# Performance work log

Hardware: AMD Instinct MI355X
Metric: run time of the kernel (lower is better)

## Reference

```python
import jax, jax.numpy as jnp
import numpy as np

HEADS = 8
DIM_HEAD = 64
SCALE = DIM_HEAD ** -0.5
LN_EPS = 1e-5
NEG_INF = -1e30


def layernorm(x, gamma, beta):
    mu = jnp.mean(x, axis=-1, keepdims=True)
    var = jnp.var(x, axis=-1, keepdims=True)
    return (x - mu) * jax.lax.rsqrt(var + LN_EPS) * gamma + beta


def setup_inputs() -> dict:
    key = jax.random.key(0)
    ks = jax.random.split(key, 8)
    b, f, n, d, inner = 8, 8192, 64, 1024, HEADS * DIM_HEAD
    x = jax.random.normal(ks[0], (b, f, d), dtype=jnp.float32)
    latents = jax.random.normal(ks[1], (b, n, d), dtype=jnp.float32)
    key_padding_mask = jax.random.randint(ks[2], (b, f), 0, 2) > 0  # True = padded
    s = 0.02
    return {
        "x": x,
        "latents": latents,
        "key_padding_mask": key_padding_mask,
        "kv_gate": jnp.float32(-4.0),
        "gamma_media": jnp.ones((d,), jnp.float32),
        "beta_media": jnp.zeros((d,), jnp.float32),
        "gamma_lat": jnp.ones((d,), jnp.float32),
        "beta_lat": jnp.zeros((d,), jnp.float32),
        "Wq": jax.random.normal(ks[3], (d, inner), jnp.float32) * s,
        "Wk": jax.random.normal(ks[4], (d, inner), jnp.float32) * s,
        "Wv": jax.random.normal(ks[5], (d, inner), jnp.float32) * s,
        "Wout": jax.random.normal(ks[6], (inner, d), jnp.float32) * s,
    }


def reference(x, latents, key_padding_mask, kv_gate, gamma_media, beta_media,
              gamma_lat, beta_lat, Wq, Wk, Wv, Wout):
    b, f, d = x.shape
    n = latents.shape[1]
    x = layernorm(x, gamma_media, beta_media)
    latents = layernorm(latents, gamma_lat, beta_lat)
    kv = jnp.concatenate((x, latents * kv_gate), axis=1)  # (b, f+n, d)

    q = (latents @ Wq).reshape(b, n, HEADS, DIM_HEAD)       # (b, q, h, d)
    k = (kv @ Wk).reshape(b, f + n, HEADS, DIM_HEAD)        # (b, kv, h, d)
    v = (kv @ Wv).reshape(b, f + n, HEADS, DIM_HEAD)

    sim = jnp.einsum('bqhd,bkhd->bhqk', q * SCALE, k)       # (b, h, n, f+n)
    sim = sim - jax.lax.stop_gradient(jnp.max(sim, axis=-1, keepdims=True))

    valid_feat = ~key_padding_mask                          # (b, f)
    valid_full = jnp.concatenate(
        (valid_feat, jnp.ones((b, n), dtype=bool)), axis=1)  # (b, f+n)
    sim = jnp.where(valid_full[:, None, None, :], sim, NEG_INF)

    attn = jax.nn.softmax(sim, axis=-1)
    out = jnp.einsum('bhqk,bkhd->bqhd', attn, v).reshape(b, n, HEADS * DIM_HEAD)
    return out @ Wout
```

## Files before the change

### kernel.cpp

```cpp
#include <hip/hip_runtime.h>
#include <stdint.h>


#define KVPAD 8448
#define NCHUNK 33

typedef __attribute__((ext_vector_type(8))) short short8;
typedef __attribute__((ext_vector_type(4))) float f32x4;

typedef __attribute__((address_space(1))) void gvoid;
typedef __attribute__((address_space(3))) void lvoid;

__device__ __forceinline__ unsigned short f2bf(float f) {
    union { float f; uint32_t u; } v; v.f = f;
    uint32_t u = v.u;
    u += 0x7fffu + ((u >> 16) & 1u);
    return (unsigned short)(u >> 16);
}

__device__ __forceinline__ void mfma16(f32x4& c, short8 a, short8 b) {
    asm volatile("v_mfma_f32_16x16x32_bf16 %0, %1, %2, %0"
                 : "+v"(c) : "v"(a), "v"(b));
}

__device__ __forceinline__ void gl2lds16(const void* g, void* l) {
    __builtin_amdgcn_global_load_lds((gvoid*)g, (lvoid*)l, 16, 0, 0);
}

__global__ __launch_bounds__(512) void scan_kernel(
    const int* __restrict__ mask, int* __restrict__ pfx, int* __restrict__ cnt)
{
    int b = threadIdx.x >> 6, lane = threadIdx.x & 63;
    int run = 0;
    for (int it = 0; it < 128; it++) {
        int f = it * 64 + lane;
        int valid = (mask[b * 8192 + f] == 0) ? 1 : 0;
        unsigned long long bal = __ballot(valid);
        int excl = __popcll(bal & ((1ull << lane) - 1ull));
        pfx[b * 8192 + f] = run + excl;
        run += (int)__popcll(bal);
    }
    if (lane == 0) cnt[b] = run;
}

__global__ __launch_bounds__(256) void ln_kernel(
    const float* __restrict__ X, const float* __restrict__ latents,
    const int* __restrict__ mask, const int* __restrict__ pfx,
    const float* __restrict__ gm, const float* __restrict__ bm,
    const float* __restrict__ gl, const float* __restrict__ bl,
    unsigned short* __restrict__ x_ln, unsigned short* __restrict__ lat_ln)
{
    int lane = threadIdx.x & 63;
    int row = blockIdx.x * 4 + (threadIdx.x >> 6);
    const float *src, *g, *bet;
    unsigned short* dst;
    if (row < 65536) {
        if (mask[row] != 0) return;
        int b = row >> 13;
        src = X + (size_t)row * 1024;
        dst = x_ln + ((size_t)b * 8192 + pfx[row]) * 1024;
        g = gm; bet = bm;
    } else {
        int r = row - 65536;
        src = latents + (size_t)r * 1024;
        dst = lat_ln + (size_t)r * 1024;
        g = gl; bet = bl;
    }
    const float4* xr = (const float4*)src;
    float4 v[4];
    float s = 0.f, s2 = 0.f;
#pragma unroll
    for (int i = 0; i < 4; i++) {
        v[i] = xr[i * 64 + lane];
        s  += v[i].x + v[i].y + v[i].z + v[i].w;
        s2 += v[i].x*v[i].x + v[i].y*v[i].y + v[i].z*v[i].z + v[i].w*v[i].w;
    }
#pragma unroll
    for (int off = 1; off < 64; off <<= 1) {
        s += __shfl_xor(s, off);
        s2 += __shfl_xor(s2, off);
    }
    float mean = s * (1.0f / 1024.0f);
    float var  = s2 * (1.0f / 1024.0f) - mean * mean;
    float rs = rsqrtf(var + 1e-5f);
    ushort4* yr = (ushort4*)dst;
    const float4* gp = (const float4*)g;
    const float4* bp = (const float4*)bet;
#pragma unroll
    for (int i = 0; i < 4; i++) {
        int c4 = i * 64 + lane;
        float4 gg = gp[c4], bb = bp[c4];
        ushort4 o;
        o.x = f2bf((v[i].x - mean) * rs * gg.x + bb.x);
        o.y = f2bf((v[i].y - mean) * rs * gg.y + bb.y);
        o.z = f2bf((v[i].z - mean) * rs * gg.z + bb.z);
        o.w = f2bf((v[i].w - mean) * rs * gg.w + bb.w);
        yr[c4] = o;
    }
}

__global__ __launch_bounds__(256) void transpose_cvt(
    const float* __restrict__ Wk, const float* __restrict__ Wv,
    const float* __restrict__ Wq, const float* __restrict__ Wout,
    unsigned short* __restrict__ WkvT, unsigned short* __restrict__ WqT,
    unsigned short* __restrict__ WoutT)
{
    __shared__ float t[64][65];
    const float* S; unsigned short* D; int R, C;
    int z = blockIdx.z;
    if (z == 0)      { S = Wk;   D = WkvT;                      R = 1024; C = 512; }
    else if (z == 1) { S = Wv;   D = WkvT + (size_t)512 * 1024; R = 1024; C = 512; }
    else if (z == 2) { S = Wq;   D = WqT;                       R = 1024; C = 512; }
    else             { S = Wout; D = WoutT;                     R = 512;  C = 1024; }
    int r0 = blockIdx.y * 64, c0 = blockIdx.x * 64;
    if (r0 >= R || c0 >= C) return;
#pragma unroll
    for (int i = 0; i < 16; i++) {
        int o = i * 256 + threadIdx.x;
        int rr = o >> 6, cc = o & 63;
        t[rr][cc] = S[(size_t)(r0 + rr) * C + c0 + cc];
    }
    __syncthreads();
#pragma unroll
    for (int i = 0; i < 16; i++) {
        int o = i * 256 + threadIdx.x;
        int cl = o >> 6, rl = o & 63;
        D[(size_t)(c0 + cl) * R + r0 + rl] = f2bf(t[rl][cl]);
    }
}

__global__ __launch_bounds__(256) void gemm_bf16(
    const unsigned short* __restrict__ A, const unsigned short* __restrict__ BT,
    int Kd,
    unsigned short* __restrict__ Ck, float* __restrict__ Cf,
    unsigned short* __restrict__ CvT,
    int nsplit, int ldc, int P, int Sstride, int Ofs, int kvpad,
    float scale_const, const float* __restrict__ scale_ptr,
    const int* __restrict__ cnt)
{
    __shared__ unsigned short a_lds[128 * 64];
    __shared__ unsigned short b_lds[128 * 64];
    int bx = blockIdx.x, by = blockIdx.y;
    if (gridDim.x == 8 && gridDim.y >= 8 && (gridDim.y & 7) == 0) {
        int lid = by * 8 + bx;
        bx = lid & 7;
        by = (lid >> 6) * 8 + ((lid >> 3) & 7);
    }
    size_t rowbase = (size_t)by * 128;
    size_t colbase = (size_t)bx * 128;
    if (cnt) {
        int bq = (int)rowbase / P, rl = (int)rowbase - bq * P;
        if (rl >= cnt[bq]) return;
    }
    int tid = threadIdx.x;
    int lane = tid & 63;
    int wave = tid >> 6;
    int wrow = (wave >> 1) * 64, wcol = (wave & 1) * 64;
    int qd = lane >> 4, cc = lane & 15;

    f32x4 acc[4][4];
#pragma unroll
    for (int mt = 0; mt < 4; mt++)
#pragma unroll
        for (int nt = 0; nt < 4; nt++)
            acc[mt][nt] = (f32x4){0.f, 0.f, 0.f, 0.f};

    int kiters = Kd >> 6;
    for (int kt = 0; kt < kiters; kt++) {
        int k0 = kt << 6;
#pragma unroll
        for (int i = 0; i < 4; i++) {
            int s = i * 256 + tid;
            int m = s >> 3, kc = s & 7;
            int kg = kc ^ (m & 7);
            gl2lds16(A + (rowbase + m) * (size_t)Kd + (k0 + kg * 8), &a_lds[s * 8]);
        }
#pragma unroll
        for (int i = 0; i < 4; i++) {
            int s = i * 256 + tid;
            int m = s >> 3, kc = s & 7;
            int kg = kc ^ (m & 7);
            gl2lds16(BT + (colbase + m) * (size_t)Kd + (k0 + kg * 8), &b_lds[s * 8]);
        }
        __syncthreads();
#pragma unroll
        for (int ks = 0; ks < 2; ks++) {
            short8 af[4], bfr[4];
            int cg = ks * 4 + qd;
#pragma unroll
            for (int mt = 0; mt < 4; mt++) {
                int m = wrow + mt * 16 + cc;
                af[mt] = *(const short8*)&a_lds[(m * 8 + (cg ^ (m & 7))) * 8];
            }
#pragma unroll
            for (int nt = 0; nt < 4; nt++) {
                int n = wcol + nt * 16 + cc;
                bfr[nt] = *(const short8*)&b_lds[(n * 8 + (cg ^ (n & 7))) * 8];
            }
#pragma unroll
            for (int mt = 0; mt < 4; mt++)
#pragma unroll
                for (int nt = 0; nt < 4; nt++)
                    mfma16(acc[mt][nt], af[mt], bfr[nt]);
        }
        __syncthreads();
    }

    float sc = scale_const;
    if (scale_ptr) sc *= *scale_ptr;
#pragma unroll
    for (int mt = 0; mt < 4; mt++) {
        int g0 = (int)rowbase + wrow + mt * 16 + qd * 4;
        int bq = g0 / P, rl = g0 - bq * P;
#pragma unroll
        for (int nt = 0; nt < 4; nt++) {
            int col = (int)colbase + wcol + nt * 16 + cc;
            if (col < nsplit) {
                int idx0 = bq * Sstride + Ofs + rl;
                if (Cf) {
#pragma unroll
                    for (int r = 0; r < 4; r++)
                        Cf[(size_t)(idx0 + r) * ldc + col] = acc[mt][nt][r] * sc;
                } else {
#pragma unroll
                    for (int r = 0; r < 4; r++)
                        Ck[(size_t)(idx0 + r) * ldc + col] = f2bf(acc[mt][nt][r] * sc);
                }
            } else {
                ushort4 pk;
                pk.x = f2bf(acc[mt][nt][0] * sc);
                pk.y = f2bf(acc[mt][nt][1] * sc);
                pk.z = f2bf(acc[mt][nt][2] * sc);
                pk.w = f2bf(acc[mt][nt][3] * sc);
                *(ushort4*)&CvT[((size_t)bq * 512 + (col - nsplit)) * kvpad + Ofs + rl] = pk;
            }
        }
    }
}

__global__ __launch_bounds__(256) void attn_kernel(
    const unsigned short* __restrict__ Kbuf,
    const unsigned short* __restrict__ Vt,
    const unsigned short* __restrict__ Qbuf,
    const int* __restrict__ cnt,
    float* __restrict__ Opart,
    float* __restrict__ Mpart,
    float* __restrict__ Lpart)
{
    __shared__ unsigned short P_lds[64 * 264];
    __shared__ float red_max[4][64];
    __shared__ float red_sum[4][64];
    __shared__ float mrow[64];

    int chunk = blockIdx.x, h = blockIdx.y, b = blockIdx.z;
    int len = 64 + cnt[b];
    int kv0 = chunk * 256;
    if (kv0 >= len) return;

    int tid = threadIdx.x, lane = tid & 63, w = tid >> 6;
    int qd = lane >> 4, cc = lane & 15;
    int pidx = (b * 8 + h) * NCHUNK + chunk;
    int kvw = kv0 + w * 64;

    short8 qf[4][2];
    const unsigned short* Qb = Qbuf + ((size_t)b * 64) * 512 + h * 64;
#pragma unroll
    for (int mt = 0; mt < 4; mt++)
#pragma unroll
        for (int ks = 0; ks < 2; ks++)
            qf[mt][ks] = *(const short8*)&Qb[(size_t)(mt * 16 + cc) * 512 + ks * 32 + qd * 8];

    f32x4 acc[4][4];
#pragma unroll
    for (int mt = 0; mt < 4; mt++)
#pragma unroll
        for (int nt = 0; nt < 4; nt++)
            acc[mt][nt] = (f32x4){0.f, 0.f, 0.f, 0.f};

    const unsigned short* Kb = Kbuf + (size_t)b * KVPAD * 512 + h * 64;
#pragma unroll
    for (int nt = 0; nt < 4; nt++) {
        int kvr = kvw + nt * 16 + cc;
#pragma unroll
        for (int ks = 0; ks < 2; ks++) {
            short8 kf = *(const short8*)&Kb[(size_t)kvr * 512 + ks * 32 + qd * 8];
#pragma unroll
            for (int mt = 0; mt < 4; mt++)
                mfma16(acc[mt][nt], qf[mt][ks], kf);
        }
    }
#pragma unroll
    for (int nt = 0; nt < 4; nt++) {
        int kv = kvw + nt * 16 + cc;
        if (kv >= len) {
#pragma unroll
            for (int mt = 0; mt < 4; mt++)
#pragma unroll
                for (int r = 0; r < 4; r++) acc[mt][nt][r] = -1e30f;
        }
    }
    float vmax[4][4];
#pragma unroll
    for (int mt = 0; mt < 4; mt++)
#pragma unroll
        for (int r = 0; r < 4; r++)
            vmax[mt][r] = fmaxf(fmaxf(acc[mt][0][r], acc[mt][1][r]),
                                fmaxf(acc[mt][2][r], acc[mt][3][r]));
#pragma unroll
    for (int off = 1; off < 16; off <<= 1)
#pragma unroll
        for (int mt = 0; mt < 4; mt++)
#pragma unroll
            for (int r = 0; r < 4; r++)
                vmax[mt][r] = fmaxf(vmax[mt][r], __shfl_xor(vmax[mt][r], off));
    if (cc == 0) {
#pragma unroll
        for (int mt = 0; mt < 4; mt++)
#pragma unroll
            for (int r = 0; r < 4; r++)
                red_max[w][mt * 16 + qd * 4 + r] = vmax[mt][r];
    }
    __syncthreads();
    if (tid < 64)
        mrow[tid] = fmaxf(fmaxf(red_max[0][tid], red_max[1][tid]),
                          fmaxf(red_max[2][tid], red_max[3][tid]));
    __syncthreads();

    float vsum[4][4];
#pragma unroll
    for (int mt = 0; mt < 4; mt++)
#pragma unroll
        for (int r = 0; r < 4; r++) {
            int row = mt * 16 + qd * 4 + r;
            float m = mrow[row];
            float ssum = 0.f;
#pragma unroll
            for (int nt = 0; nt < 4; nt++) {
                float p = __expf(acc[mt][nt][r] - m);
                ssum += p;
                P_lds[row * 264 + w * 64 + nt * 16 + cc] = f2bf(p);
            }
            vsum[mt][r] = ssum;
        }
#pragma unroll
    for (int off = 1; off < 16; off <<= 1)
#pragma unroll
        for (int mt = 0; mt < 4; mt++)
#pragma unroll
            for (int r = 0; r < 4; r++)
                vsum[mt][r] += __shfl_xor(vsum[mt][r], off);
    if (cc == 0) {
#pragma unroll
        for (int mt = 0; mt < 4; mt++)
#pragma unroll
            for (int r = 0; r < 4; r++)
                red_sum[w][mt * 16 + qd * 4 + r] = vsum[mt][r];
    }
    __syncthreads();
    if (tid < 64) {
        Mpart[(size_t)pidx * 64 + tid] = mrow[tid];
        Lpart[(size_t)pidx * 64 + tid] = red_sum[0][tid] + red_sum[1][tid] +
                                         red_sum[2][tid] + red_sum[3][tid];
    }

    f32x4 acco[4];
#pragma unroll
    for (int mt = 0; mt < 4; mt++) acco[mt] = (f32x4){0.f, 0.f, 0.f, 0.f};
    const unsigned short* Vb = Vt + ((size_t)b * 512 + h * 64 + w * 16 + cc) * KVPAD + kv0;
#pragma unroll
    for (int ks = 0; ks < 8; ks++) {
        short8 vf = *(const short8*)&Vb[ks * 32 + qd * 8];
#pragma unroll
        for (int mt = 0; mt < 4; mt++) {
            short8 pf = *(const short8*)&P_lds[(size_t)(mt * 16 + cc) * 264 + ks * 32 + qd * 8];
            mfma16(acco[mt], pf, vf);
        }
    }
    float* Ob = Opart + (size_t)pidx * 4096;
#pragma unroll
    for (int mt = 0; mt < 4; mt++)
#pragma unroll
        for (int r = 0; r < 4; r++)
            Ob[(size_t)(mt * 16 + qd * 4 + r) * 64 + w * 16 + cc] = acco[mt][r];
}

__global__ __launch_bounds__(256) void combine_kernel(
    const float* __restrict__ Opart, const float* __restrict__ Mpart,
    const float* __restrict__ Lpart, const int* __restrict__ cnt,
    unsigned short* __restrict__ AttnOut)
{
    __shared__ float wls[NCHUNK][16];
    __shared__ float invl[16];
    int bh = blockIdx.x >> 2, qg = blockIdx.x & 3;
    int b = bh >> 3, h = bh & 7;
    int pbase = bh * NCHUNK;
    int nact = (64 + cnt[b] + 255) >> 8;
    int tid = threadIdx.x;
    if (tid < 16) {
        int q = qg * 16 + tid;
        float M = -3.0e38f;
        for (int cn = 0; cn < nact; cn++)
            M = fmaxf(M, Mpart[(size_t)(pbase + cn) * 64 + q]);
        float l = 0.f;
        for (int cn = 0; cn < nact; cn++) {
            float wc = __expf(Mpart[(size_t)(pbase + cn) * 64 + q] - M);
            wls[cn][tid] = wc;
            l += wc * Lpart[(size_t)(pbase + cn) * 64 + q];
        }
        invl[tid] = 1.0f / l;
    }
    __syncthreads();
    int ql = tid >> 4, d4 = (tid & 15) * 4;
    int q = qg * 16 + ql;
    float ax = 0.f, ay = 0.f, az = 0.f, aw = 0.f;
    for (int cn = 0; cn < nact; cn++) {
        float wc = wls[cn][ql];
        float4 o = *(const float4*)&Opart[((size_t)(pbase + cn) * 64 + q) * 64 + d4];
        ax += wc * o.x; ay += wc * o.y; az += wc * o.z; aw += wc * o.w;
    }
    float iv = invl[ql];
    ushort4 pk;
    pk.x = f2bf(ax * iv); pk.y = f2bf(ay * iv);
    pk.z = f2bf(az * iv); pk.w = f2bf(aw * iv);
    *(ushort4*)&AttnOut[((size_t)b * 64 + q) * 512 + h * 64 + d4] = pk;
}

#define OPART_OFF    ((size_t)0)
#define MPART_OFF    ((size_t)34603008)
#define LPART_OFF    ((size_t)35143680)
#define QBUF_OFF     ((size_t)35684352)
#define ATTNOUT_OFF  ((size_t)36208640)
#define XLN_OFF      ((size_t)0)
#define LATLN_OFF    ((size_t)134217728)
#define KBUF_OFF     ((size_t)135266304)
#define VT_OFF       ((size_t)204472320)
#define WKVT_OFF     ((size_t)273678336)
#define WQT_OFF      ((size_t)275775488)
#define WOUTT_OFF    ((size_t)276824064)
#define PFX_OFF      ((size_t)277872640)
#define CNT_OFF      ((size_t)278134784)

extern "C" void kernel_launch(void* const* d_in, const int* in_sizes, int n_in,
                              void* d_out, int out_size, void* d_ws, size_t ws_size,
                              hipStream_t stream) {
    const float* x       = (const float*)d_in[0];
    const float* latents = (const float*)d_in[1];
    const int*   mask    = (const int*)d_in[2];
    const float* kv_gate = (const float*)d_in[3];
    const float* gm      = (const float*)d_in[4];
    const float* bm      = (const float*)d_in[5];
    const float* gl      = (const float*)d_in[6];
    const float* bl      = (const float*)d_in[7];
    const float* Wq      = (const float*)d_in[8];
    const float* Wk      = (const float*)d_in[9];
    const float* Wv      = (const float*)d_in[10];
    const float* Wout    = (const float*)d_in[11];
    float* out = (float*)d_out;

    char* ws = (char*)d_ws;
    float* Opart = (float*)(ws + OPART_OFF);
    float* Mpart = (float*)(ws + MPART_OFF);
    float* Lpart = (float*)(ws + LPART_OFF);
    unsigned short* Qbuf    = (unsigned short*)(ws + QBUF_OFF);
    unsigned short* AttnOut = (unsigned short*)(ws + ATTNOUT_OFF);
    unsigned short* x_ln    = (unsigned short*)(ws + XLN_OFF);
    unsigned short* lat_ln  = (unsigned short*)(ws + LATLN_OFF);
    unsigned short* Kbuf    = (unsigned short*)(ws + KBUF_OFF);
    unsigned short* Vt      = (unsigned short*)(ws + VT_OFF);
    unsigned short* WkvT    = (unsigned short*)(ws + WKVT_OFF);
    unsigned short* WqT     = (unsigned short*)(ws + WQT_OFF);
    unsigned short* WoutT   = (unsigned short*)(ws + WOUTT_OFF);
    int* pfx = (int*)(ws + PFX_OFF);
    int* cnt = (int*)(ws + CNT_OFF);

    scan_kernel<<<1, 512, 0, stream>>>(mask, pfx, cnt);

    ln_kernel<<<16512, 256, 0, stream>>>(x, latents, mask, pfx,
                                         gm, bm, gl, bl, x_ln, lat_ln);

    transpose_cvt<<<dim3(16, 16, 4), 256, 0, stream>>>(
        Wk, Wv, Wq, Wout, WkvT, WqT, WoutT);

    gemm_bf16<<<dim3(8, 512), 256, 0, stream>>>(
        x_ln, WkvT, 1024, Kbuf, nullptr, Vt,
        512, 512, 8192, KVPAD, 64, KVPAD, 1.0f, nullptr, cnt);

    gemm_bf16<<<dim3(8, 4), 256, 0, stream>>>(
        lat_ln, WkvT, 1024, Kbuf, nullptr, Vt,
        512, 512, 64, KVPAD, 0, KVPAD, 1.0f, kv_gate, nullptr);

    gemm_bf16<<<dim3(4, 4), 256, 0, stream>>>(
        lat_ln, WqT, 1024, Qbuf, nullptr, nullptr,
        1 << 30, 512, 64, 64, 0, KVPAD, 0.125f, nullptr, nullptr);

    attn_kernel<<<dim3(NCHUNK, 8, 8), 256, 0, stream>>>(
        Kbuf, Vt, Qbuf, cnt, Opart, Mpart, Lpart);

    combine_kernel<<<256, 256, 0, stream>>>(Opart, Mpart, Lpart, cnt, AttnOut);

    gemm_bf16<<<dim3(8, 4), 256, 0, stream>>>(
        AttnOut, WoutT, 512, nullptr, out, nullptr,
        1 << 30, 1024, 64, 64, 0, KVPAD, 1.0f, nullptr, nullptr);
}
```

Measured before the change: 553.2 us.

## Merge scan, layernorm and weight transpose into one prep kernel with atomic compaction

Replaces the single-block prefix-scan kernel with per-row atomicAdd slot assignment inside the layernorm kernel. The weight transpose/convert blocks are appended to the same grid, and the latent K/V and Q projections are fused into one GEMM launch. This removes a serial single-workgroup scan and several small launches. In exchange, compacted row order becomes nondeterministic and a memset is added to zero the counters.

New measurement: 834.8 us. 1.51x slower.

```diff
diff --git a/kernel.cpp b/kernel.cpp
--- a/kernel.cpp
+++ b/kernel.cpp
@@ -27,38 +27,55 @@
     __builtin_amdgcn_global_load_lds((gvoid*)g, (lvoid*)l, 16, 0, 0);
 }
 
-__global__ __launch_bounds__(512) void scan_kernel(
-    const int* __restrict__ mask, int* __restrict__ pfx, int* __restrict__ cnt)
-{
-    int b = threadIdx.x >> 6, lane = threadIdx.x & 63;
-    int run = 0;
-    for (int it = 0; it < 128; it++) {
-        int f = it * 64 + lane;
-        int valid = (mask[b * 8192 + f] == 0) ? 1 : 0;
-        unsigned long long bal = __ballot(valid);
-        int excl = __popcll(bal & ((1ull << lane) - 1ull));
-        pfx[b * 8192 + f] = run + excl;
-        run += (int)__popcll(bal);
-    }
-    if (lane == 0) cnt[b] = run;
-}
-
-__global__ __launch_bounds__(256) void ln_kernel(
+__global__ __launch_bounds__(256) void prep_kernel(
     const float* __restrict__ X, const float* __restrict__ latents,
-    const int* __restrict__ mask, const int* __restrict__ pfx,
+    const int* __restrict__ mask,
     const float* __restrict__ gm, const float* __restrict__ bm,
     const float* __restrict__ gl, const float* __restrict__ bl,
-    unsigned short* __restrict__ x_ln, unsigned short* __restrict__ lat_ln)
+    const float* __restrict__ Wk, const float* __restrict__ Wv,
+    const float* __restrict__ Wq, const float* __restrict__ Wout,
+    unsigned short* __restrict__ x_ln, unsigned short* __restrict__ lat_ln,
+    unsigned short* __restrict__ WkvqT, unsigned short* __restrict__ WoutT,
+    int* __restrict__ cnt)
 {
+    __shared__ float t[64][65];
+    int blk = blockIdx.x;
+    if (blk >= 16512) {
+        int tt = blk - 16512;
+        int z = tt >> 7, u = tt & 127;
+        const float* S; unsigned short* D; int R, C, bx, by;
+        if (z == 0)      { S = Wk;   D = WkvqT;                       R = 1024; C = 512;  by = u >> 3; bx = u & 7; }
+        else if (z == 1) { S = Wv;   D = WkvqT + (size_t)512 * 1024;  R = 1024; C = 512;  by = u >> 3; bx = u & 7; }
+        else if (z == 2) { S = Wq;   D = WkvqT + (size_t)1024 * 1024; R = 1024; C = 512;  by = u >> 3; bx = u & 7; }
+        else             { S = Wout; D = WoutT;                       R = 512;  C = 1024; by = u >> 4; bx = u & 15; }
+        int r0 = by * 64, c0 = bx * 64;
+#pragma unroll
+        for (int i = 0; i < 16; i++) {
+            int o = i * 256 + threadIdx.x;
+            int rr = o >> 6, cc = o & 63;
+            t[rr][cc] = S[(size_t)(r0 + rr) * C + c0 + cc];
+        }
+        __syncthreads();
+#pragma unroll
+        for (int i = 0; i < 16; i++) {
+            int o = i * 256 + threadIdx.x;
+            int cl = o >> 6, rl = o & 63;
+            D[(size_t)(c0 + cl) * R + r0 + rl] = f2bf(t[rl][cl]);
+        }
+        return;
+    }
     int lane = threadIdx.x & 63;
-    int row = blockIdx.x * 4 + (threadIdx.x >> 6);
+    int row = blk * 4 + (threadIdx.x >> 6);
     const float *src, *g, *bet;
     unsigned short* dst;
     if (row < 65536) {
         if (mask[row] != 0) return;
         int b = row >> 13;
+        int slot;
+        if (lane == 0) slot = atomicAdd(&cnt[b], 1);
+        slot = __shfl(slot, 0);
         src = X + (size_t)row * 1024;
-        dst = x_ln + ((size_t)b * 8192 + pfx[row]) * 1024;
+        dst = x_ln + ((size_t)b * 8192 + slot) * 1024;
         g = gm; bet = bm;
     } else {
         int r = row - 65536;
@@ -99,49 +116,19 @@
     }
 }
 
-__global__ __launch_bounds__(256) void transpose_cvt(
-    const float* __restrict__ Wk, const float* __restrict__ Wv,
-    const float* __restrict__ Wq, const float* __restrict__ Wout,
-    unsigned short* __restrict__ WkvT, unsigned short* __restrict__ WqT,
-    unsigned short* __restrict__ WoutT)
-{
-    __shared__ float t[64][65];
-    const float* S; unsigned short* D; int R, C;
-    int z = blockIdx.z;
-    if (z == 0)      { S = Wk;   D = WkvT;                      R = 1024; C = 512; }
-    else if (z == 1) { S = Wv;   D = WkvT + (size_t)512 * 1024; R = 1024; C = 512; }
-    else if (z == 2) { S = Wq;   D = WqT;                       R = 1024; C = 512; }
-    else             { S = Wout; D = WoutT;                     R = 512;  C = 1024; }
-    int r0 = blockIdx.y * 64, c0 = blockIdx.x * 64;
-    if (r0 >= R || c0 >= C) return;
-#pragma unroll
-    for (int i = 0; i < 16; i++) {
-        int o = i * 256 + threadIdx.x;
-        int rr = o >> 6, cc = o & 63;
-        t[rr][cc] = S[(size_t)(r0 + rr) * C + c0 + cc];
-    }
-    __syncthreads();
-#pragma unroll
-    for (int i = 0; i < 16; i++) {
-        int o = i * 256 + threadIdx.x;
-        int cl = o >> 6, rl = o & 63;
-        D[(size_t)(c0 + cl) * R + r0 + rl] = f2bf(t[rl][cl]);
-    }
-}
-
 __global__ __launch_bounds__(256) void gemm_bf16(
     const unsigned short* __restrict__ A, const unsigned short* __restrict__ BT,
     int Kd,
     unsigned short* __restrict__ Ck, float* __restrict__ Cf,
-    unsigned short* __restrict__ CvT,
-    int nsplit, int ldc, int P, int Sstride, int Ofs, int kvpad,
-    float scale_const, const float* __restrict__ scale_ptr,
+    unsigned short* __restrict__ CvT, unsigned short* __restrict__ Qb,
+    int nsplit, int nq, int ldc, int P, int Sstride, int Ofs,
+    float scale_const, float qscale, const float* __restrict__ scale_ptr,
     const int* __restrict__ cnt)
 {
     __shared__ unsigned short a_lds[128 * 64];
     __shared__ unsigned short b_lds[128 * 64];
     int bx = blockIdx.x, by = blockIdx.y;
-    if (gridDim.x == 8 && gridDim.y >= 8 && (gridDim.y & 7) == 0) {
+    if (gridDim.x == 8 && gridDim.y >= 8) {
         int lid = by * 8 + bx;
         bx = lid & 7;
         by = (lid >> 6) * 8 + ((lid >> 3) & 7);
@@ -215,7 +202,12 @@
 #pragma unroll
         for (int nt = 0; nt < 4; nt++) {
             int col = (int)colbase + wcol + nt * 16 + cc;
-            if (col < nsplit) {
+            if (col >= nq) {
+#pragma unroll
+                for (int r = 0; r < 4; r++)
+                    Qb[(size_t)(bq * 64 + rl + r) * 512 + (col - nq)] =
+                        f2bf(acc[mt][nt][r] * qscale);
+            } else if (col < nsplit) {
                 int idx0 = bq * Sstride + Ofs + rl;
                 if (Cf) {
 #pragma unroll
@@ -232,7 +224,7 @@
                 pk.y = f2bf(acc[mt][nt][1] * sc);
                 pk.z = f2bf(acc[mt][nt][2] * sc);
                 pk.w = f2bf(acc[mt][nt][3] * sc);
-                *(ushort4*)&CvT[((size_t)bq * 512 + (col - nsplit)) * kvpad + Ofs + rl] = pk;
+                *(ushort4*)&CvT[((size_t)bq * 512 + (col - nsplit)) * KVPAD + Ofs + rl] = pk;
             }
         }
     }
@@ -434,11 +426,9 @@
 #define LATLN_OFF    ((size_t)134217728)
 #define KBUF_OFF     ((size_t)135266304)
 #define VT_OFF       ((size_t)204472320)
-#define WKVT_OFF     ((size_t)273678336)
-#define WQT_OFF      ((size_t)275775488)
+#define WKVQT_OFF    ((size_t)273678336)
 #define WOUTT_OFF    ((size_t)276824064)
-#define PFX_OFF      ((size_t)277872640)
-#define CNT_OFF      ((size_t)278134784)
+#define CNT_OFF      ((size_t)277872640)
 
 extern "C" void kernel_launch(void* const* d_in, const int* in_sizes, int n_in,
                               void* d_out, int out_size, void* d_ws, size_t ws_size,
@@ -467,31 +457,23 @@
     unsigned short* lat_ln  = (unsigned short*)(ws + LATLN_OFF);
     unsigned short* Kbuf    = (unsigned short*)(ws + KBUF_OFF);
     unsigned short* Vt      = (unsigned short*)(ws + VT_OFF);
-    unsigned short* WkvT    = (unsigned short*)(ws + WKVT_OFF);
-    unsigned short* WqT     = (unsigned short*)(ws + WQT_OFF);
+    unsigned short* WkvqT   = (unsigned short*)(ws + WKVQT_OFF);
     unsigned short* WoutT   = (unsigned short*)(ws + WOUTT_OFF);
-    int* pfx = (int*)(ws + PFX_OFF);
     int* cnt = (int*)(ws + CNT_OFF);
 
-    scan_kernel<<<1, 512, 0, stream>>>(mask, pfx, cnt);
-
-    ln_kernel<<<16512, 256, 0, stream>>>(x, latents, mask, pfx,
-                                         gm, bm, gl, bl, x_ln, lat_ln);
-
-    transpose_cvt<<<dim3(16, 16, 4), 256, 0, stream>>>(
-        Wk, Wv, Wq, Wout, WkvT, WqT, WoutT);
+    hipMemsetAsync(cnt, 0, 8 * sizeof(int), stream);
+
+    prep_kernel<<<17024, 256, 0, stream>>>(
+        x, latents, mask, gm, bm, gl, bl, Wk, Wv, Wq, Wout,
+        x_ln, lat_ln, WkvqT, WoutT, cnt);
 
     gemm_bf16<<<dim3(8, 512), 256, 0, stream>>>(
-        x_ln, WkvT, 1024, Kbuf, nullptr, Vt,
-        512, 512, 8192, KVPAD, 64, KVPAD, 1.0f, nullptr, cnt);
-
-    gemm_bf16<<<dim3(8, 4), 256, 0, stream>>>(
-        lat_ln, WkvT, 1024, Kbuf, nullptr, Vt,
-        512, 512, 64, KVPAD, 0, KVPAD, 1.0f, kv_gate, nullptr);
-
-    gemm_bf16<<<dim3(4, 4), 256, 0, stream>>>(
-        lat_ln, WqT, 1024, Qbuf, nullptr, nullptr,
-        1 << 30, 512, 64, 64, 0, KVPAD, 0.125f, nullptr, nullptr);
+        x_ln, WkvqT, 1024, Kbuf, nullptr, Vt, nullptr,
+        512, 1 << 30, 512, 8192, KVPAD, 64, 1.0f, 0.f, nullptr, cnt);
+
+    gemm_bf16<<<dim3(12, 4), 256, 0, stream>>>(
+        lat_ln, WkvqT, 1024, Kbuf, nullptr, Vt, Qbuf,
+        512, 1024, 512, 64, KVPAD, 0, 1.0f, 0.125f, kv_gate, nullptr);
 
     attn_kernel<<<dim3(NCHUNK, 8, 8), 256, 0, stream>>>(
         Kbuf, Vt, Qbuf, cnt, Opart, Mpart, Lpart);
@@ -499,6 +481,6 @@
     combine_kernel<<<256, 256, 0, stream>>>(Opart, Mpart, Lpart, cnt, AttnOut);
 
     gemm_bf16<<<dim3(8, 4), 256, 0, stream>>>(
-        AttnOut, WoutT, 512, nullptr, out, nullptr,
-        1 << 30, 1024, 64, 64, 0, KVPAD, 1.0f, nullptr, nullptr);
-}
+        AttnOut, WoutT, 512, nullptr, out, nullptr, nullptr,
+        1 << 30, 1 << 30, 1024, 64, 64, 0, 1.0f, 0.f, nullptr, nullptr);
+}
```
